# Kernel tuning notes

Hardware: AMD Instinct MI355X
Metric: run time of the kernel (lower is better)

Reference implementation:

```python
import jax, jax.numpy as jnp
import numpy as np

NUM_SPLITS = 4
SPLIT_CH = 4          # 16 channels / 4 splits
N_BRANCH = NUM_SPLITS * 2   # 2 pyramid branches per group
K = 2                 # multi_frequency_compression k
MAX_U, MAX_V = 5, 5
N_CLASSES = 60
LN_EPS = 1e-5


def _conv(x, w):
    # x: [B, Cin, H, W], w: [Cout, Cin, kh, kw], SAME padding, stride 1
    return jax.lax.conv_general_dilated(
        x, w, window_strides=(1, 1), padding='SAME',
        dimension_numbers=('NCHW', 'OIHW', 'NCHW'))


def _branch(x, w3, b3, w5, b5, w7, b7):
    # one PyramidMultiScaleCNN branch: dense 3x3 -> 5x5 -> 7x7 with input re-concat
    a = jax.nn.relu(_conv(x, w3) + b3[None, :, None, None])            # [B,64,H,W]
    b = jax.nn.relu(_conv(jnp.concatenate([a, x], 1), w5) + b5[None, :, None, None])  # [B,128,H,W]
    c = jax.nn.relu(_conv(jnp.concatenate([b, x], 1), w7) + b7[None, :, None, None])  # [B,256,H,W]
    return jnp.concatenate([a, b, c], axis=1)                          # [B,448,H,W]


def _dct_basis(H, W, dtype):
    # first K frequency pairs (u,v) in row-major order of a MAX_U x MAX_V grid
    uv = [(i // MAX_V, i % MAX_V) for i in range(K)]
    u = jnp.array([p[0] for p in uv], dtype=dtype)   # [K]
    v = jnp.array([p[1] for p in uv], dtype=dtype)   # [K]
    h = jnp.arange(H, dtype=dtype) + 0.5
    w = jnp.arange(W, dtype=dtype) + 0.5
    cos_u = jnp.cos(jnp.pi * u[:, None] * h[None, :] / H)  # [K,H]
    cos_v = jnp.cos(jnp.pi * v[:, None] * w[None, :] / W)  # [K,W]
    return cos_u, cos_v


def setup_inputs() -> dict:
    key = jax.random.key(0)
    ks = jax.random.split(key, 16)
    B, C, H, W = 16, 16, 32, 32
    s = 0.02
    x = jax.random.normal(ks[0], (B, C, H, W), jnp.float32)
    # stacked params for the 8 identical-shaped pyramid branches (index = 2*group + branch)
    w3 = jax.random.normal(ks[1], (N_BRANCH, 64, SPLIT_CH, 3, 3), jnp.float32) * s
    b3 = jnp.zeros((N_BRANCH, 64), jnp.float32)
    w5 = jax.random.normal(ks[2], (N_BRANCH, 128, 64 + SPLIT_CH, 5, 5), jnp.float32) * s
    b5 = jnp.zeros((N_BRANCH, 128), jnp.float32)
    w7 = jax.random.normal(ks[3], (N_BRANCH, 256, 128 + SPLIT_CH, 7, 7), jnp.float32) * s
    b7 = jnp.zeros((N_BRANCH, 256), jnp.float32)
    fused_c = N_BRANCH * 448  # 3584
    Wg = jax.random.normal(ks[4], (N_CLASSES, fused_c), jnp.float32) * s
    bg = jnp.zeros((N_CLASSES,), jnp.float32)
    f_dct = fused_c * K       # 7168
    gamma = jnp.ones((f_dct,), jnp.float32)
    beta = jnp.zeros((f_dct,), jnp.float32)
    Wd = jax.random.normal(ks[5], (N_CLASSES, f_dct), jnp.float32) * s
    bd = jnp.zeros((N_CLASSES,), jnp.float32)
    return {"x": x, "w3": w3, "b3": b3, "w5": w5, "b5": b5, "w7": w7, "b7": b7,
            "Wg": Wg, "bg": bg, "gamma": gamma, "beta": beta, "Wd": Wd, "bd": bd}


def reference(x, w3, b3, w5, b5, w7, b7, Wg, bg, gamma, beta, Wd, bd):
    B, C, H, W = x.shape
    # split channels into groups: [NUM_SPLITS, B, SPLIT_CH, H, W]
    parts = x.reshape(B, NUM_SPLITS, SPLIT_CH, H, W).transpose(1, 0, 2, 3, 4)
    # each group feeds 2 branches; branch index i = 2*group + branch matches fused cat order
    xg = jnp.repeat(parts, 2, axis=0)                               # [8,B,SPLIT_CH,H,W]
    outs = jax.vmap(_branch)(xg, w3, b3, w5, b5, w7, b7)            # [8,B,448,H,W]
    fused = outs.transpose(1, 0, 2, 3, 4).reshape(B, N_BRANCH * 448, H, W)  # [B,3584,H,W]

    # GAP head
    gap_feat = fused.mean(axis=(2, 3))                              # [B,3584]
    gap_pred = gap_feat @ Wg.T + bg                                 # [B,60]

    # batched multi-frequency DCT compression (replaces per-sample Python loop)
    cos_u, cos_v = _dct_basis(H, W, fused.dtype)                    # [K,H],[K,W]
    dct = jnp.einsum('bchw,kh,kw->bck', fused, cos_u, cos_v)        # [B,3584,K]
    dct = dct.reshape(B, -1)                                        # [B,7168]

    mu = dct.mean(axis=-1, keepdims=True)
    var = jnp.var(dct, axis=-1, keepdims=True)
    normed = (dct - mu) * jax.lax.rsqrt(var + LN_EPS) * gamma + beta
    # dropout omitted (eval mode)
    dct_pred = normed @ Wd.T + bd                                   # [B,60]
    return (gap_pred, dct_pred)
```

## Files before the change

### kernel.cpp

```cpp
#include <hip/hip_runtime.h>
#include <math.h>

#define PI_F 3.14159265358979323846f

typedef short bf16x8 __attribute__((ext_vector_type(8)));
typedef float f32x4  __attribute__((ext_vector_type(4)));
typedef float f32x16 __attribute__((ext_vector_type(16)));

__device__ __forceinline__ short f2bf(float f) {
    union { float f; unsigned u; } v; v.f = f;
    unsigned r = v.u + 0x7fffu + ((v.u >> 16) & 1u);
    return (short)(r >> 16);
}

__device__ __forceinline__ void gld16(const short* g, short* l) {
    __builtin_amdgcn_global_load_lds(
        (const __attribute__((address_space(1))) unsigned int*)g,
        (__attribute__((address_space(3))) unsigned int*)l, 16, 0, 0);
}


__global__ __launch_bounds__(256) void prep_s1in(const float* __restrict__ x, short* __restrict__ dst) {
    int idx = blockIdx.x * 256 + threadIdx.x;
    if (idx >= 64 * 1024) return;
    int px = idx & 1023;
    int g  = (idx >> 10) & 3;
    int b  = idx >> 12;
    short v8[8];
    #pragma unroll
    for (int j = 0; j < 8; ++j) {
        float f = (j < 4) ? x[((b * 16 + g * 4 + j) << 10) + px] : 0.f;
        v8[j] = f2bf(f);
    }
    *(int4*)(dst + (size_t)idx * 8) = *(const int4*)v8;
}

__global__ __launch_bounds__(256) void prep_sx(const float* __restrict__ x, short* __restrict__ dst,
                                               int CHS, int CH0) {
    int idx = blockIdx.x * 256 + threadIdx.x;
    if (idx >= 128 * 1024) return;
    int px = idx & 1023, pair = idx >> 10;
    int i = pair >> 4, b = pair & 15, g = i >> 1;
    short v8[8];
    #pragma unroll
    for (int j = 0; j < 8; ++j) {
        float f = (j < 4) ? x[((b * 16 + g * 4 + j) << 10) + px] : 0.f;
        v8[j] = f2bf(f);
    }
    *(int4*)(dst + (size_t)idx * CHS + CH0) = *(const int4*)v8;
}

__global__ __launch_bounds__(256) void prep_s3x(const float* __restrict__ x, short* __restrict__ dst) {
    int idx = blockIdx.x * 256 + threadIdx.x;
    if (idx >= 128 * 1024) return;
    int px = idx & 1023, pair = idx >> 10;
    int i = pair >> 4, b = pair & 15, g = i >> 1;
    int R = px >> 5, C = px & 31;
    short v8[8];
    #pragma unroll
    for (int j = 0; j < 8; ++j) {
        float f = (j < 4) ? x[((b * 16 + g * 4 + j) << 10) + px] : 0.f;
        v8[j] = f2bf(f);
    }
    int p = ((C + 3) * 136 + 128) * 2;
    p ^= ((p >> 7) & 1) << 4;
    *(int4*)((char*)dst + ((size_t)pair * 38 + R + 3) * 11264 + p) = *(const int4*)v8;
}

template<int KS, int CHS, int CINR, int COUT, int NCH>
__global__ __launch_bounds__(256) void wprep_d(const float* __restrict__ w, short* __restrict__ Bw) {
    constexpr int TOTAL = 8 * KS * NCH * COUT * 4;
    int idx = blockIdx.x * 256 + threadIdx.x;
    if (idx >= TOTAL) return;
    int kb = idx & 3;
    int r  = idx >> 2;
    int n  = r % COUT;  r /= COUT;
    int c  = r % NCH;   r /= NCH;
    int kh = r % KS;
    int br = r / KS;
    short v8[8];
    #pragma unroll
    for (int j = 0; j < 8; ++j) {
        int k   = c * 32 + kb * 8 + j;
        int kwc = k / CHS;
        int ch  = k - kwc * CHS;
        float f = (kwc < KS && ch < CINR)
                ? w[(((size_t)br * COUT + n) * CINR + ch) * (KS * KS) + kh * KS + kwc] : 0.f;
        v8[j] = f2bf(f);
    }
    *(int4*)(Bw + (size_t)idx * 8) = *(const int4*)v8;
}

template<int KS, int CHS, int COUT, int CHS_OUT, int FOFF, bool S1SRC, bool POUT>
__global__ __launch_bounds__(512, 2) void conv_hk(
    const short* __restrict__ sIn,
    short* __restrict__ sOut,
    const short* __restrict__ Bw,
    const float* __restrict__ bias,
    float* __restrict__ sums)
{
    constexpr int PAD    = KS / 2;
    constexpr int NCH    = (KS * CHS + 31) / 32;
    constexpr int TCX    = 32 + (NCH * 32 - 1) / CHS;
    constexpr int NSLOT  = 9;
    constexpr int NFN    = COUT / 64;
    constexpr int CPP    = CHS / 8;
    constexpr int RCHK   = TCX * CPP;
    constexpr int CHUNKB = COUT * 32;
    static_assert(NCH == 1 || (NCH % 2) == 0, "NCH must be 1 or even");
    static_assert(RCHK <= 512, "single stg reg");

    __shared__ int4 AtileV[(NSLOT * TCX * CHS) / 8];
    short* Atile = (short*)AtileV;

    const int t    = threadIdx.x;
    const int lane = t & 63, w = t >> 6;
    const int wm = w >> 2, wn = w & 3;
    const int lm = lane & 15, kb = lane >> 4;

    const int bid = blockIdx.x;
    const int i  = bid & 7;
    const int b  = (bid >> 3) & 15;
    const int mt = bid >> 7;
    const int r0 = mt * 8;

    const int pairIdx = i * 16 + b;
    const int pairPx = pairIdx << 10;
    const int srcPx  = S1SRC ? ((b * 4 + (i >> 1)) << 10) : pairPx;

    int nIdx[NFN], nOff[NFN];
    #pragma unroll
    for (int fn = 0; fn < NFN; ++fn) {
        nIdx[fn] = wn * (COUT / 4) + fn * 16 + lm;
        nOff[fn] = nIdx[fn] * 32 + kb * 8;
    }

    f32x4 acc[8][NFN];
    #pragma unroll
    for (int fm = 0; fm < 8; ++fm)
        #pragma unroll
        for (int fn = 0; fn < NFN; ++fn)
            acc[fm][fn] = (f32x4){0.f, 0.f, 0.f, 0.f};

    const short* Bp = Bw + (size_t)i * KS * NCH * CHUNKB;
    bf16x8 b0[NFN], b1[NFN];
    #pragma unroll
    for (int fn = 0; fn < NFN; ++fn)
        b0[fn] = *(const bf16x8*)(Bp + nOff[fn]);

    for (int e = t; e < 9 * RCHK; e += 512) {
        int j  = e / RCHK, e2 = e - j * RCHK;
        int tc = e2 / CPP, kc = e2 - tc * CPP;
        int rin = r0 - PAD + j, cin = tc - PAD;
        int4 v = {0, 0, 0, 0};
        if (rin >= 0 && rin < 32 && cin >= 0 && cin < 32)
            v = *(const int4*)(sIn + (size_t)(srcPx + rin * 32 + cin) * CHS + kc * 8);
        *(int4*)(Atile + (j * TCX + tc) * CHS + kc * 8) = v;
    }
    __syncthreads();

    int aB[8];

    for (int kh = 0; kh < KS; ++kh) {
        #pragma unroll
        for (int fm = 0; fm < 8; ++fm) {
            int slot = kh + wm * 4 + (fm >> 1);
            if (slot >= NSLOT) slot -= NSLOT;
            aB[fm] = (slot * TCX + (fm & 1) * 16 + lm) * CHS + kb * 8;
        }

        const bool doStage = (kh <= KS - 3);
        const int stRin = r0 - PAD + kh + 9;
        int4 stg0 = {0, 0, 0, 0};
        if (doStage) {
            if (t < RCHK) {
                int tc = t / CPP, kc = t - tc * CPP;
                int cin = tc - PAD;
                if (stRin >= 0 && stRin < 32 && cin >= 0 && cin < 32)
                    stg0 = *(const int4*)(sIn + (size_t)(srcPx + stRin * 32 + cin) * CHS + kc * 8);
            }
        }

        if constexpr (NCH == 1) {
            __builtin_amdgcn_s_setprio(1);
            #pragma unroll
            for (int fm = 0; fm < 8; ++fm) {
                bf16x8 af = *(const bf16x8*)(Atile + aB[fm]);
                #pragma unroll
                for (int fn = 0; fn < NFN; ++fn)
                    acc[fm][fn] = __builtin_amdgcn_mfma_f32_16x16x32_bf16(af, b0[fn], acc[fm][fn], 0, 0, 0);
            }
            __builtin_amdgcn_s_setprio(0);
            if (kh < KS - 1) {
                #pragma unroll
                for (int fn = 0; fn < NFN; ++fn)
                    b0[fn] = *(const bf16x8*)(Bp + CHUNKB + nOff[fn]);
            }
            Bp += CHUNKB;
        } else {
            #pragma unroll 1
            for (int c = 0; c < NCH; c += 2) {
                #pragma unroll
                for (int fn = 0; fn < NFN; ++fn)
                    b1[fn] = *(const bf16x8*)(Bp + (size_t)(c + 1) * CHUNKB + nOff[fn]);
                __builtin_amdgcn_s_setprio(1);
                #pragma unroll
                for (int fm = 0; fm < 8; ++fm) {
                    bf16x8 af = *(const bf16x8*)(Atile + aB[fm] + c * 32);
                    #pragma unroll
                    for (int fn = 0; fn < NFN; ++fn)
                        acc[fm][fn] = __builtin_amdgcn_mfma_f32_16x16x32_bf16(af, b0[fn], acc[fm][fn], 0, 0, 0);
                }
                __builtin_amdgcn_s_setprio(0);
                if (!(kh == KS - 1 && c + 2 >= NCH)) {
                    #pragma unroll
                    for (int fn = 0; fn < NFN; ++fn)
                        b0[fn] = *(const bf16x8*)(Bp + (size_t)(c + 2) * CHUNKB + nOff[fn]);
                }
                __builtin_amdgcn_s_setprio(1);
                #pragma unroll
                for (int fm = 0; fm < 8; ++fm) {
                    bf16x8 af = *(const bf16x8*)(Atile + aB[fm] + (c + 1) * 32);
                    #pragma unroll
                    for (int fn = 0; fn < NFN; ++fn)
                        acc[fm][fn] = __builtin_amdgcn_mfma_f32_16x16x32_bf16(af, b1[fn], acc[fm][fn], 0, 0, 0);
                }
                __builtin_amdgcn_s_setprio(0);
            }
            Bp += (size_t)NCH * CHUNKB;
        }

        __syncthreads();
        if (doStage && t < RCHK) {
            int tc = t / CPP, kc = t - tc * CPP;
            *(int4*)(Atile + (kh * TCX + tc) * CHS + kc * 8) = stg0;
        }
    }

    float cwv[2][4];
    #pragma unroll
    for (int half = 0; half < 2; ++half)
        #pragma unroll
        for (int r = 0; r < 4; ++r)
            cwv[half][r] = cosf(PI_F * (half * 16 + kb * 4 + r + 0.5f) / 32.f);

    #pragma unroll
    for (int fn = 0; fn < NFN; ++fn) {
        int n = nIdx[fn];
        float bv = bias[i * COUT + n];
        float s0 = 0.f, s1 = 0.f;
        #pragma unroll
        for (int fm = 0; fm < 8; ++fm) {
            int imgrow = wm * 4 + (fm >> 1);
            int half = fm & 1;
            #pragma unroll
            for (int r = 0; r < 4; ++r) {
                float v = fmaxf(acc[fm][fn][r] + bv, 0.f);
                int col = half * 16 + kb * 4 + r;
                int R = r0 + imgrow;
                if constexpr (POUT) {
                    int p = ((col + 3) * CHS_OUT + n) * 2;
                    p ^= ((p >> 7) & 1) << 4;
                    *(short*)((char*)sOut + ((size_t)pairIdx * 38 + R + 3) * 11264 + p) = f2bf(v);
                } else if constexpr (CHS_OUT > 0) {
                    sOut[(size_t)(pairPx + R * 32 + col) * CHS_OUT + n] = f2bf(v);
                }
                s0 += v;
                s1 += v * cwv[half][r];
            }
        }
        s0 += __shfl_xor(s0, 16); s1 += __shfl_xor(s1, 16);
        s0 += __shfl_xor(s0, 32); s1 += __shfl_xor(s1, 32);
        if (kb == 0) {
            int ch = i * 448 + FOFF + n;
            atomicAdd(&sums[((size_t)b * 3584 + ch) * 2 + 0], s0);
            atomicAdd(&sums[((size_t)b * 3584 + ch) * 2 + 1], s1);
        }
    }
}

__global__ __launch_bounds__(512, 2) void conv7_fused(
    const short* __restrict__ sPad,
    const short* __restrict__ Bw,
    const float* __restrict__ bias,
    float* __restrict__ sums)
{
    constexpr int NCH = 30, COUT = 256;
    constexpr int RSTR = 5632;
    constexpr int CHUNKB = COUT * 32;

    __shared__ int4 AldsV[(14 * RSTR) / 8];
    short* Alds = (short*)AldsV;

    const int t    = threadIdx.x;
    const int lane = t & 63, w = t >> 6;
    const int ln = lane & 31, hi = lane >> 5;

    const int bid = blockIdx.x;
    const int i  = bid & 7;
    const int b  = (bid >> 3) & 15;
    const int mt = bid >> 7;
    const int r0 = mt * 8;
    const size_t sBase = (size_t)(i * 16 + b) * 38 * RSTR;

    const int n = w * 32 + ln;
    const int nOffB = n * 32 + hi * 8;

    f32x16 acc[8];
    #pragma unroll
    for (int ro = 0; ro < 8; ++ro) acc[ro] = (f32x16)(0.f);

    const short* BpI = Bw + (size_t)i * 7 * NCH * CHUNKB;

    for (int s = w; s < 154; s += 8) {
        int j = s / 11, sg = s - j * 11;
        gld16(sPad + sBase + (size_t)(r0 + j) * RSTR + sg * 512 + lane * 8,
              Alds + j * RSTR + sg * 512 + lane * 8);
    }
    bf16x8 bA[7], bB[7];
    #pragma unroll
    for (int kh = 0; kh < 7; ++kh)
        bA[kh] = *(const bf16x8*)(BpI + (size_t)kh * NCH * CHUNKB + nOffB);
    __syncthreads();

    auto HALF = [&](bf16x8 (&bq)[7], int c, int kk) {
        int swb = ln * 272 + c * 64 + kk * 32 + hi * 16;
        swb ^= ((swb >> 7) & 1) << 4;
        #pragma unroll
        for (int j = 0; j < 14; ++j) {
            bf16x8 af = *(const bf16x8*)((const char*)Alds + j * 11264 + swb);
            const int klo = (j > 7) ? (j - 7) : 0;
            const int khi = (j < 6) ? j : 6;
            #pragma unroll
            for (int kh = klo; kh <= khi; ++kh)
                acc[j - kh] = __builtin_amdgcn_mfma_f32_32x32x16_bf16(af, bq[kh], acc[j - kh], 0, 0, 0);
        }
    };

    #pragma unroll 1
    for (int c = 0; c < NCH; ++c) {
        #pragma unroll
        for (int kh = 0; kh < 7; ++kh)
            bB[kh] = *(const bf16x8*)(BpI + ((size_t)kh * NCH + c) * CHUNKB + nOffB + 16);
        HALF(bA, c, 0);
        if (c + 1 < NCH) {
            #pragma unroll
            for (int kh = 0; kh < 7; ++kh)
                bA[kh] = *(const bf16x8*)(BpI + ((size_t)kh * NCH + c + 1) * CHUNKB + nOffB);
        }
        HALF(bB, c, 1);
    }

    float cw[16];
    #pragma unroll
    for (int r = 0; r < 16; ++r) {
        int px = (r & 3) + 8 * (r >> 2) + 4 * hi;
        cw[r] = cosf(PI_F * (px + 0.5f) / 32.f);
    }

    float bv = bias[i * COUT + n];
    float s0 = 0.f, s1 = 0.f;
    #pragma unroll
    for (int ro = 0; ro < 8; ++ro) {
        #pragma unroll
        for (int r = 0; r < 16; ++r) {
            float v = fmaxf(acc[ro][r] + bv, 0.f);
            s0 += v;
            s1 += v * cw[r];
        }
    }
    s0 += __shfl_xor(s0, 32);
    s1 += __shfl_xor(s1, 32);
    if (hi == 0) {
        int ch = i * 448 + 192 + n;
        atomicAdd(&sums[((size_t)b * 3584 + ch) * 2 + 0], s0);
        atomicAdd(&sums[((size_t)b * 3584 + ch) * 2 + 1], s1);
    }
}

__global__ __launch_bounds__(256) void ln_stats(const float* __restrict__ sums,
                                                float* __restrict__ stats) {
    __shared__ float red[8];
    const int b = blockIdx.x;
    const int t = threadIdx.x, lane = t & 63, wv = t >> 6;
    const float* S = sums + (size_t)b * 7168;
    float ls = 0.f, lq = 0.f;
    for (int f = t; f < 7168; f += 256) { float v = S[f]; ls += v; lq += v * v; }
    for (int m = 1; m < 64; m <<= 1) { ls += __shfl_xor(ls, m); lq += __shfl_xor(lq, m); }
    if (lane == 0) { red[wv] = ls; red[4 + wv] = lq; }
    __syncthreads();
    if (t == 0) {
        float ts = red[0] + red[1] + red[2] + red[3];
        float tq = red[4] + red[5] + red[6] + red[7];
        float mu  = ts * (1.f / 7168.f);
        float var = tq * (1.f / 7168.f) - mu * mu;
        stats[b * 2 + 0] = mu;
        stats[b * 2 + 1] = rsqrtf(var + 1e-5f);
    }
}

__global__ __launch_bounds__(256) void head_gemv(
    const float* __restrict__ sums,
    const float* __restrict__ stats,
    const float* __restrict__ Wg, const float* __restrict__ bg,
    const float* __restrict__ gamma, const float* __restrict__ beta,
    const float* __restrict__ Wd, const float* __restrict__ bd,
    float* __restrict__ out)
{
    __shared__ float red[8];
    const int n = blockIdx.x % 60;
    const int b = blockIdx.x / 60;
    const int t = threadIdx.x, lane = t & 63, wv = t >> 6;
    const float* S  = sums + (size_t)b * 7168;
    const float mu  = stats[b * 2 + 0];
    const float inv = stats[b * 2 + 1];

    const float* wd = Wd + (size_t)n * 7168;
    float accd = 0.f;
    for (int f = t; f < 7168; f += 256) {
        float v = (S[f] - mu) * inv * gamma[f] + beta[f];
        accd = fmaf(v, wd[f], accd);
    }
    const float* wg = Wg + (size_t)n * 3584;
    float accg = 0.f;
    for (int ch = t; ch < 3584; ch += 256)
        accg = fmaf(S[2 * ch], wg[ch], accg);

    for (int m = 1; m < 64; m <<= 1) { accg += __shfl_xor(accg, m); accd += __shfl_xor(accd, m); }
    if (lane == 0) { red[wv] = accg; red[4 + wv] = accd; }
    __syncthreads();
    if (t == 0) {
        float g = red[0] + red[1] + red[2] + red[3];
        float d = red[4] + red[5] + red[6] + red[7];
        out[b * 60 + n]       = g * (1.f / 1024.f) + bg[n];
        out[960 + b * 60 + n] = d + bd[n];
    }
}

extern "C" void kernel_launch(void* const* d_in, const int* in_sizes, int n_in,
                              void* d_out, int out_size, void* d_ws, size_t ws_size,
                              hipStream_t stream)
{
    const float* x     = (const float*)d_in[0];
    const float* w3    = (const float*)d_in[1];
    const float* b3    = (const float*)d_in[2];
    const float* w5    = (const float*)d_in[3];
    const float* b5    = (const float*)d_in[4];
    const float* w7    = (const float*)d_in[5];
    const float* b7    = (const float*)d_in[6];
    const float* Wg    = (const float*)d_in[7];
    const float* bg    = (const float*)d_in[8];
    const float* gamma = (const float*)d_in[9];
    const float* beta  = (const float*)d_in[10];
    const float* Wd    = (const float*)d_in[11];
    const float* bd    = (const float*)d_in[12];
    float* out = (float*)d_out;

    char* p = (char*)d_ws;
    float* sums  = (float*)p;             p += 458752;
    float* stats = (float*)p;             p += 128;
    short* s1in  = (short*)p;             p += 1048576;
    short* s2in  = (short*)p;             p += 18874368;
    short* s3pad = (short*)p;             p += 54788096;
    short* Bw3   = (short*)p;             p += 98304;
    short* Bw5   = (short*)p;             p += 3932160;
    short* Bw7   = (short*)p;             p += 27525120;

    hipMemsetAsync(sums, 0, 458752, stream);
    hipMemsetAsync(s3pad, 0, 54788096, stream);
    prep_s1in<<<dim3(256), dim3(256), 0, stream>>>(x, s1in);
    prep_sx<<<dim3(512), dim3(256), 0, stream>>>(x, s2in, 72, 64);
    prep_s3x<<<dim3(512), dim3(256), 0, stream>>>(x, s3pad);
    wprep_d<3, 8, 4, 64, 1><<<dim3(24), dim3(256), 0, stream>>>(w3, Bw3);
    wprep_d<5, 72, 68, 128, 12><<<dim3(960), dim3(256), 0, stream>>>(w5, Bw5);
    wprep_d<7, 136, 132, 256, 30><<<dim3(6720), dim3(256), 0, stream>>>(w7, Bw7);

    conv_hk<3, 8, 64, 72, 0, true, false><<<dim3(512), dim3(512), 0, stream>>>(s1in, s2in, Bw3, b3, sums);
    conv_hk<5, 72, 128, 136, 64, false, true><<<dim3(512), dim3(512), 0, stream>>>(s2in, s3pad, Bw5, b5, sums);
    conv7_fused<<<dim3(512), dim3(512), 0, stream>>>(s3pad, Bw7, b7, sums);

    ln_stats<<<dim3(16), dim3(256), 0, stream>>>(sums, stats);
    head_gemv<<<dim3(960), dim3(256), 0, stream>>>(sums, stats, Wg, bg, gamma, beta, Wd, bd, out);
}
```

Before: 488.9 us.

## Split conv7 rows across two wave groups with 1024-thread blocks

The 7x7 conv kernel now runs 16 waves per block instead of 8. Each half of the block computes 4 of the 8 output rows, which halves the accumulator registers per wave, and the 7 filter rows are split into two register groups that are prefetched in a staggered way. s_setprio is raised around the MFMA bursts. This is meant to add more resident waves and better hide the latency of the global weight loads, at the cost of loading each weight fragment twice (once per row group) and more LDS read traffic per block.

```diff
diff --git a/kernel.cpp b/kernel.cpp
--- a/kernel.cpp
+++ b/kernel.cpp
@@ -279,7 +279,7 @@
     }
 }
 
-__global__ __launch_bounds__(512, 2) void conv7_fused(
+__global__ __launch_bounds__(1024, 4) void conv7_fused(
     const short* __restrict__ sPad,
     const short* __restrict__ Bw,
     const float* __restrict__ bias,
@@ -294,7 +294,10 @@
 
     const int t    = threadIdx.x;
     const int lane = t & 63, w = t >> 6;
+    const int g  = w >> 3;
+    const int wn = w & 7;
     const int ln = lane & 31, hi = lane >> 5;
+    const int m0 = g * 4;
 
     const int bid = blockIdx.x;
     const int i  = bid & 7;
@@ -303,52 +306,70 @@
     const int r0 = mt * 8;
     const size_t sBase = (size_t)(i * 16 + b) * 38 * RSTR;
 
-    const int n = w * 32 + ln;
+    const int n = wn * 32 + ln;
     const int nOffB = n * 32 + hi * 8;
 
-    f32x16 acc[8];
-    #pragma unroll
-    for (int ro = 0; ro < 8; ++ro) acc[ro] = (f32x16)(0.f);
+    f32x16 acc[4];
+    #pragma unroll
+    for (int d = 0; d < 4; ++d) acc[d] = (f32x16)(0.f);
 
     const short* BpI = Bw + (size_t)i * 7 * NCH * CHUNKB;
 
-    for (int s = w; s < 154; s += 8) {
+    bf16x8 bq0[4], bq1[3];
+    auto LDB0 = [&](int h2) {
+        int c2 = h2 >> 1, kk2 = h2 & 1;
+        #pragma unroll
+        for (int kh = 0; kh < 4; ++kh)
+            bq0[kh] = *(const bf16x8*)(BpI + ((size_t)kh * NCH + c2) * CHUNKB + nOffB + kk2 * 16);
+    };
+    auto LDB1 = [&](int h2) {
+        int c2 = h2 >> 1, kk2 = h2 & 1;
+        #pragma unroll
+        for (int kh = 4; kh < 7; ++kh)
+            bq1[kh - 4] = *(const bf16x8*)(BpI + ((size_t)kh * NCH + c2) * CHUNKB + nOffB + kk2 * 16);
+    };
+
+    LDB0(0); LDB1(0);
+
+    for (int s = w; s < 154; s += 16) {
         int j = s / 11, sg = s - j * 11;
         gld16(sPad + sBase + (size_t)(r0 + j) * RSTR + sg * 512 + lane * 8,
               Alds + j * RSTR + sg * 512 + lane * 8);
     }
-    bf16x8 bA[7], bB[7];
-    #pragma unroll
-    for (int kh = 0; kh < 7; ++kh)
-        bA[kh] = *(const bf16x8*)(BpI + (size_t)kh * NCH * CHUNKB + nOffB);
     __syncthreads();
 
-    auto HALF = [&](bf16x8 (&bq)[7], int c, int kk) {
-        int swb = ln * 272 + c * 64 + kk * 32 + hi * 16;
-        swb ^= ((swb >> 7) & 1) << 4;
-        #pragma unroll
-        for (int j = 0; j < 14; ++j) {
-            bf16x8 af = *(const bf16x8*)((const char*)Alds + j * 11264 + swb);
-            const int klo = (j > 7) ? (j - 7) : 0;
-            const int khi = (j < 6) ? j : 6;
+    #pragma unroll 1
+    for (int h = 0; h < 60; ++h) {
+        const int c = h >> 1, kk = h & 1;
+        int sw = ln * 272 + c * 64 + kk * 32 + hi * 16;
+        sw ^= ((sw >> 7) & 1) << 4;
+        const char* Ab = (const char*)Alds + m0 * 11264 + sw;
+
+        __builtin_amdgcn_s_setprio(1);
+        #pragma unroll
+        for (int jp = 0; jp <= 6; ++jp) {
+            bf16x8 af = *(const bf16x8*)(Ab + jp * 11264);
+            const int klo = (jp > 3) ? (jp - 3) : 0;
+            const int khi = (jp < 3) ? jp : 3;
             #pragma unroll
             for (int kh = klo; kh <= khi; ++kh)
-                acc[j - kh] = __builtin_amdgcn_mfma_f32_32x32x16_bf16(af, bq[kh], acc[j - kh], 0, 0, 0);
-        }
-    };
-
-    #pragma unroll 1
-    for (int c = 0; c < NCH; ++c) {
-        #pragma unroll
-        for (int kh = 0; kh < 7; ++kh)
-            bB[kh] = *(const bf16x8*)(BpI + ((size_t)kh * NCH + c) * CHUNKB + nOffB + 16);
-        HALF(bA, c, 0);
-        if (c + 1 < NCH) {
+                acc[jp - kh] = __builtin_amdgcn_mfma_f32_32x32x16_bf16(af, bq0[kh], acc[jp - kh], 0, 0, 0);
+        }
+        __builtin_amdgcn_s_setprio(0);
+        if (h < 59) LDB0(h + 1);
+
+        __builtin_amdgcn_s_setprio(1);
+        #pragma unroll
+        for (int jp = 4; jp <= 9; ++jp) {
+            bf16x8 af = *(const bf16x8*)(Ab + jp * 11264);
+            const int klo = (jp - 3 > 4) ? (jp - 3) : 4;
+            const int khi = (jp < 6) ? jp : 6;
             #pragma unroll
-            for (int kh = 0; kh < 7; ++kh)
-                bA[kh] = *(const bf16x8*)(BpI + ((size_t)kh * NCH + c + 1) * CHUNKB + nOffB);
-        }
-        HALF(bB, c, 1);
+            for (int kh = klo; kh <= khi; ++kh)
+                acc[jp - kh] = __builtin_amdgcn_mfma_f32_32x32x16_bf16(af, bq1[kh - 4], acc[jp - kh], 0, 0, 0);
+        }
+        __builtin_amdgcn_s_setprio(0);
+        if (h < 59) LDB1(h + 1);
     }
 
     float cw[16];
@@ -361,10 +382,10 @@
     float bv = bias[i * COUT + n];
     float s0 = 0.f, s1 = 0.f;
     #pragma unroll
-    for (int ro = 0; ro < 8; ++ro) {
+    for (int d = 0; d < 4; ++d) {
         #pragma unroll
         for (int r = 0; r < 16; ++r) {
-            float v = fmaxf(acc[ro][r] + bv, 0.f);
+            float v = fmaxf(acc[d][r] + bv, 0.f);
             s0 += v;
             s1 += v * cw[r];
         }
@@ -477,7 +498,7 @@
 
     conv_hk<3, 8, 64, 72, 0, true, false><<<dim3(512), dim3(512), 0, stream>>>(s1in, s2in, Bw3, b3, sums);
     conv_hk<5, 72, 128, 136, 64, false, true><<<dim3(512), dim3(512), 0, stream>>>(s2in, s3pad, Bw5, b5, sums);
-    conv7_fused<<<dim3(512), dim3(512), 0, stream>>>(s3pad, Bw7, b7, sums);
+    conv7_fused<<<dim3(512), dim3(1024), 0, stream>>>(s3pad, Bw7, b7, sums);
 
     ln_stats<<<dim3(16), dim3(256), 0, stream>>>(sums, stats);
     head_gemv<<<dim3(960), dim3(256), 0, stream>>>(sums, stats, Wg, bg, gamma, beta, Wd, bd, out);
```

Result: slower. 546.2 us (+11.7%).
